# Kernel optimization log

Measured on AMD Instinct MI355X. Metric: run time of the kernel, lower is better.

Reference implementation:

```python
import jax, jax.numpy as jnp
import numpy as np
import math

B, LQ, LK = 8, 1024, 1024
DQ = DK = DV = DOUT = 512
H = 8
DH = DOUT // H
EPS = 1e-5


def _ln(x, g, b):
    m = jnp.mean(x, -1, keepdims=True)
    var = jnp.mean((x - m) ** 2, -1, keepdims=True)
    return (x - m) * jax.lax.rsqrt(var + EPS) * g + b


def setup_inputs() -> dict:
    key = jax.random.key(0)
    ks = jax.random.split(key, 13)
    s = 0.02
    return {
        "q": jax.random.normal(ks[0], (B, LQ, DQ), jnp.float32),
        "k": jax.random.normal(ks[1], (B, LK, DK), jnp.float32),
        "v": jax.random.normal(ks[2], (B, LK, DV), jnp.float32),
        "mask": jax.random.randint(ks[3], (B, LK), 0, 2) > 0,  # True = masked
        "Wq": jax.random.normal(ks[4], (DOUT, DQ), jnp.float32) * s,
        "Wk": jax.random.normal(ks[5], (DOUT, DK), jnp.float32) * s,
        "Wv": jax.random.normal(ks[6], (DOUT, DV), jnp.float32) * s,
        "Wo": jax.random.normal(ks[7], (DOUT, DOUT), jnp.float32) * s,
        "bo": jnp.zeros((DOUT,), jnp.float32),
        "g1": jnp.ones((DOUT,), jnp.float32),
        "b1": jnp.zeros((DOUT,), jnp.float32),
        "g2": jnp.ones((DOUT,), jnp.float32),
        "b2": jnp.zeros((DOUT,), jnp.float32),
    }


def reference(q, k, v, mask, Wq, Wk, Wv, Wo, bo, g1, b1, g2, b2):
    qp = q @ Wq.T  # [B,Lq,D]
    kp = k @ Wk.T  # [B,Lk,D]
    vp = v @ Wv.T  # [B,Lk,D]

    # split heads: chunk(num_heads, -1) -> head h = contiguous slice of size DH
    qh = qp.reshape(B, LQ, H, DH)
    kh = kp.reshape(B, LK, H, DH)
    vh = vp.reshape(B, LK, H, DH)

    # NOTE: module divides by sqrt(dim_out), not sqrt(head_dim)
    logits = jnp.einsum("bqhd,bkhd->bhqk", qh, kh) / math.sqrt(DOUT)
    logits = jnp.where(mask[:, None, None, :], -jnp.inf, logits)
    A = jax.nn.softmax(logits, axis=-1)
    A = jnp.where(jnp.isnan(A), 0.0, A)  # masked_fill(isnan, 0)

    attn = jnp.einsum("bhqk,bkhd->bqhd", A, vh).reshape(B, LQ, DOUT)

    out = _ln(qp + attn, g1, b1)
    out = _ln(out + jax.nn.relu(out @ Wo.T + bo), g2, b2)
    return out
```

## Files before the change

kernel.cpp:

```cpp
#include <hip/hip_runtime.h>
#include <math.h>
#include <stdint.h>

#define NB 8
#define SEQ 1024
#define DMODEL 512
#define NH 8
#define HD 64
#define R_TOT (NB * SEQ)

typedef __attribute__((ext_vector_type(8))) short bf16x8;
typedef __attribute__((ext_vector_type(4))) float f32x4;

__device__ __forceinline__ short f2b(float x) {
    uint32_t u = __float_as_uint(x);
    u += 0x7FFF + ((u >> 16) & 1);
    return (short)(u >> 16);
}
__device__ __forceinline__ float b2f(short s) {
    return __uint_as_float(((uint32_t)(uint16_t)s) << 16);
}
__device__ __forceinline__ uint32_t cvtpk_bf16(float lo, float hi) {
    uint32_t r;
    asm("v_cvt_pk_bf16_f32 %0, %1, %2" : "=v"(r) : "v"(lo), "v"(hi));
    return r;
}
__device__ __forceinline__ float exp2_hw(float x) {
    float r;
    asm("v_exp_f32 %0, %1" : "=v"(r) : "v"(x));
    return r;
}

#define GLD_LDS16(g, l)                                                        \
    __builtin_amdgcn_global_load_lds(                                          \
        (const __attribute__((address_space(1))) uint32_t*)(g),                \
        (__attribute__((address_space(3))) uint32_t*)(l), 16, 0, 0)

__device__ __forceinline__ void xcd_swizzle(int& bx, int& by, int& bz) {
    const int gx = gridDim.x, gy = gridDim.y;
    const int nwg = gx * gy * gridDim.z;
    int id = (blockIdx.z * gy + blockIdx.y) * gx + blockIdx.x;
    int lg = (id & 7) * (nwg >> 3) + (id >> 3);
    bx = lg % gx;
    int tmp = lg / gx;
    by = tmp % gy;
    bz = tmp / gy;
}

#define N4B (R_TOT * DMODEL / 4)
#define N4W (DMODEL * DMODEL / 4)

__global__ __launch_bounds__(256)
void cvt_all(const float* __restrict__ q, const float* __restrict__ k, const float* __restrict__ v,
             const float* __restrict__ wq, const float* __restrict__ wk,
             const float* __restrict__ wv, const float* __restrict__ wo,
             short* dq, short* dk, short* dv, short* dwq, short* dwk, short* dwv, short* dwo)
{
    long i = (long)blockIdx.x * 256 + threadIdx.x;
    const float* s; short* d; long off;
    if (i < (long)N4B)          { s = q;  d = dq;  off = i; }
    else if (i < 2L * N4B)      { s = k;  d = dk;  off = i - N4B; }
    else if (i < 3L * N4B)      { s = v;  d = dv;  off = i - 2L * N4B; }
    else {
        long j = i - 3L * N4B;
        int  w = (int)(j >> 16);
        off = j & (N4W - 1);
        s = (w == 0) ? wq : (w == 1) ? wk : (w == 2) ? wv : wo;
        d = (w == 0) ? dwq : (w == 1) ? dwk : (w == 2) ? dwv : dwo;
    }
    float4 x = ((const float4*)s)[off];
    short4 o;
    o.x = f2b(x.x); o.y = f2b(x.y); o.z = f2b(x.z); o.w = f2b(x.w);
    ((short4*)d)[off] = o;
}

#define GBM 128
#define GBN 64
#define GBK 64

__device__ __forceinline__ void gemm_core(
    const short* __restrict__ A, const short* __restrict__ Bm,
    const float* __restrict__ bias, short* __restrict__ C,
    int N, int m0, int n0, int relu, float oscale,
    short (*As)[GBM * GBK], short (*Bs)[GBN * GBK])
{
    const int tid = threadIdx.x;
    const int l   = tid & 63, w = tid >> 6;
    const int l15 = l & 15,  l4 = l >> 4;
    const int wrow = w >> 1, wcol = w & 1;
    const int K = 512;

    f32x4 acc[4][2] = {};

    auto stageA = [&](int t, int buf) {
        #pragma unroll
        for (int j = 0; j < 4; ++j) {
            int ch  = tid + j * 256;
            int row = ch >> 3;
            int so  = (((ch & 7) * 16) ^ ((row & 7) << 4)) >> 1;
            GLD_LDS16(A + (size_t)(m0 + row) * K + t * GBK + so, &As[buf][ch * 8]);
        }
    };
    auto stageB = [&](int t, int buf) {
        #pragma unroll
        for (int j = 0; j < 2; ++j) {
            int ch  = tid + j * 256;
            int row = ch >> 3;
            int so  = (((ch & 7) * 16) ^ ((row & 7) << 4)) >> 1;
            GLD_LDS16(Bm + (size_t)(n0 + row) * K + t * GBK + so, &Bs[buf][ch * 8]);
        }
    };

    stageA(0, 0); stageB(0, 0);
    __syncthreads();

    for (int t = 0; t < 8; ++t) {
        const int cur = t & 1;
        if (t + 1 < 8) { stageA(t + 1, cur ^ 1); stageB(t + 1, cur ^ 1); }
        __builtin_amdgcn_s_setprio(1);
        #pragma unroll
        for (int kk = 0; kk < 2; ++kk) {
            bf16x8 af[4], bfr[2];
            #pragma unroll
            for (int mi = 0; mi < 4; ++mi) {
                int row = wrow * 64 + mi * 16 + l15;
                af[mi] = *(const bf16x8*)((char*)&As[cur][row * GBK] +
                                          ((kk * 64 + l4 * 16) ^ ((row & 7) << 4)));
            }
            #pragma unroll
            for (int ni = 0; ni < 2; ++ni) {
                int row = wcol * 32 + ni * 16 + l15;
                bfr[ni] = *(const bf16x8*)((char*)&Bs[cur][row * GBK] +
                                           ((kk * 64 + l4 * 16) ^ ((row & 7) << 4)));
            }
            #pragma unroll
            for (int mi = 0; mi < 4; ++mi)
                #pragma unroll
                for (int ni = 0; ni < 2; ++ni)
                    acc[mi][ni] = __builtin_amdgcn_mfma_f32_16x16x32_bf16(af[mi], bfr[ni], acc[mi][ni], 0, 0, 0);
        }
        __builtin_amdgcn_s_setprio(0);
        __syncthreads();
    }

    #pragma unroll
    for (int mi = 0; mi < 4; ++mi) {
        #pragma unroll
        for (int ni = 0; ni < 2; ++ni) {
            int col = n0 + wcol * 32 + ni * 16 + l15;
            float bb = bias ? bias[col] : 0.0f;
            #pragma unroll
            for (int r = 0; r < 4; ++r) {
                int row = m0 + wrow * 64 + mi * 16 + l4 * 4 + r;
                float vv = (acc[mi][ni][r] + bb) * oscale;
                if (relu) vv = fmaxf(vv, 0.0f);
                C[(size_t)row * N + col] = f2b(vv);
            }
        }
    }
}

__global__ __launch_bounds__(256)
void proj3(const short* __restrict__ qb, const short* __restrict__ kb,
           const short* __restrict__ vb, const short* __restrict__ wq,
           const short* __restrict__ wv,
           short* __restrict__ qpb, short* __restrict__ vtb, float kscale)
{
    __shared__ short As[2][GBM * GBK];
    __shared__ short Bs[2][GBN * GBK];
    const size_t WSZ  = (size_t)DMODEL * DMODEL;
    const size_t SLOT = (size_t)R_TOT * DMODEL;

    int id = blockIdx.x;
    int lg = (id & 7) * 192 + (id >> 3);

    const short *A, *Bm; short* C; int N, m0, n0; float os = 1.0f;
    if (lg < 1024) {
        int bz  = lg >> 9;
        int rem = lg & 511;
        m0 = (rem >> 3) * GBM;
        n0 = (rem & 7) * GBN;
        A  = bz ? kb : qb;
        Bm = wq + bz * WSZ;
        C  = qpb + bz * SLOT;
        N  = DMODEL;
        os = bz ? kscale : 1.0f;
    } else {
        int r2  = lg - 1024;
        int b   = r2 >> 6;
        int rem = r2 & 63;
        m0 = (rem >> 4) * GBM;
        n0 = (rem & 15) * GBN;
        A  = wv;
        Bm = vb + (long)b * SEQ * DMODEL;
        C  = vtb + (long)b * DMODEL * SEQ;
        N  = SEQ;
    }
    gemm_core(A, Bm, nullptr, C, N, m0, n0, 0, os, As, Bs);
}

__global__ __launch_bounds__(256)
void outproj(const short* __restrict__ y, const short* __restrict__ wo,
             const float* __restrict__ bias, short* __restrict__ z)
{
    __shared__ short As[2][GBM * GBK];
    __shared__ short Bs[2][GBN * GBK];
    int bx, by, bz;
    xcd_swizzle(bx, by, bz);
    gemm_core(y, wo, bias, z, DMODEL, by * GBM, bx * GBN, 1, 1.0f, As, Bs);
}

__global__ __launch_bounds__(512)
void attn_mfma8(const short* __restrict__ qp, const short* __restrict__ kp,
                const short* __restrict__ vt, const int* __restrict__ mask,
                short* __restrict__ attn)
{
    __shared__ short Kb[2][2][64 * 64];
    __shared__ short Vb[2][2][64 * 64];
    __shared__ __align__(16) char Ps[8 * 2048];

    const int tid = threadIdx.x;
    const int l   = tid & 63, w = tid >> 6;
    const int l15 = l & 15,  l4 = l >> 4;
    int qb_, h, b;
    xcd_swizzle(qb_, h, b);
    const int qrow = qb_ * 128 + w * 16 + l15;
    const size_t baseqk = ((size_t)b * SEQ) * DMODEL + h * HD;
    const size_t basev  = ((size_t)b * DMODEL + h * HD) * SEQ;

    const int ch  = tid;
    const int row = ch >> 3;
    const int so  = ((((ch & 7) * 16) ^ ((row & 7) << 4)) >> 1);
    const short* kph = kp + baseqk;
    const short* vth = vt + basev;
    const int*   mrow = mask + b * SEQ;

#define STAGE(t, bufi) do {                                                                   \
        GLD_LDS16(kph + (size_t)((t) * 128 + row) * DMODEL + so,      &Kb[bufi][0][ch * 8]);  \
        GLD_LDS16(kph + (size_t)((t) * 128 + 64 + row) * DMODEL + so, &Kb[bufi][1][ch * 8]);  \
        GLD_LDS16(vth + (size_t)row * SEQ + (t) * 128 + so,           &Vb[bufi][0][ch * 8]);  \
        GLD_LDS16(vth + (size_t)row * SEQ + (t) * 128 + 64 + so,      &Vb[bufi][1][ch * 8]);  \
    } while (0)

    const int swk   = (l15 & 7) << 4;
    const int kOff0 = l15 * 128 + ((l4 * 16) ^ swk);
    const int kOff1 = l15 * 128 + ((64 + l4 * 16) ^ swk);
    int pwOff[4];
    #pragma unroll
    for (int c = 0; c < 4; ++c)
        pwOff[c] = (l15 * 128 + c * 32 + l4 * 8) ^ swk;
    const int prOff0 = (l15 * 128 + l4 * 16) ^ swk;
    const int prOff1 = (l15 * 128 + 64 + l4 * 16) ^ swk;

    bf16x8 qf0, qf1;
    {
        const short* qr = qp + baseqk + (size_t)qrow * DMODEL + l4 * 8;
        qf0 = *(const bf16x8*)qr;
        qf1 = *(const bf16x8*)(qr + 32);
    }
    const bf16x8 ones = {0x3F80, 0x3F80, 0x3F80, 0x3F80, 0x3F80, 0x3F80, 0x3F80, 0x3F80};

    STAGE(0, 0);
    __syncthreads();

    f32x4 oacc[4] = {};
    f32x4 osum = {};
    char* myPs = Ps + w * 2048;

    for (int t = 0; t < 8; ++t) {
        const int cur = t & 1;
        if (t < 7) STAGE(t + 1, cur ^ 1);

        #pragma unroll
        for (int hf = 0; hf < 2; ++hf) {
            f32x4 s[4];
            __builtin_amdgcn_s_setprio(1);
            #pragma unroll
            for (int c = 0; c < 4; ++c) {
                const char* kbase = (const char*)&Kb[cur][hf][0] + c * 2048;
                bf16x8 kf0 = *(const bf16x8*)(kbase + kOff0);
                bf16x8 kf1 = *(const bf16x8*)(kbase + kOff1);
                f32x4 zz = {};
                zz = __builtin_amdgcn_mfma_f32_16x16x32_bf16(kf0, qf0, zz, 0, 0, 0);
                zz = __builtin_amdgcn_mfma_f32_16x16x32_bf16(kf1, qf1, zz, 0, 0, 0);
                s[c] = zz;
            }
            __builtin_amdgcn_s_setprio(0);

            float p[16];
            #pragma unroll
            for (int c = 0; c < 4; ++c) {
                int4 mi = *(const int4*)&mrow[t * 128 + hf * 64 + c * 16 + l4 * 4];
                p[c * 4 + 0] = exp2_hw(mi.x ? -1.0e30f : s[c][0]);
                p[c * 4 + 1] = exp2_hw(mi.y ? -1.0e30f : s[c][1]);
                p[c * 4 + 2] = exp2_hw(mi.z ? -1.0e30f : s[c][2]);
                p[c * 4 + 3] = exp2_hw(mi.w ? -1.0e30f : s[c][3]);
            }

            #pragma unroll
            for (int c = 0; c < 4; ++c) {
                uint2 u;
                u.x = cvtpk_bf16(p[c * 4 + 0], p[c * 4 + 1]);
                u.y = cvtpk_bf16(p[c * 4 + 2], p[c * 4 + 3]);
                *(uint2*)(myPs + pwOff[c]) = u;
            }
            bf16x8 pf0 = *(const bf16x8*)(myPs + prOff0);
            bf16x8 pf1 = *(const bf16x8*)(myPs + prOff1);

            __builtin_amdgcn_s_setprio(1);
            osum = __builtin_amdgcn_mfma_f32_16x16x32_bf16(ones, pf0, osum, 0, 0, 0);
            osum = __builtin_amdgcn_mfma_f32_16x16x32_bf16(ones, pf1, osum, 0, 0, 0);
            #pragma unroll
            for (int db = 0; db < 4; ++db) {
                const char* vbase = (const char*)&Vb[cur][hf][0] + db * 2048;
                bf16x8 vf0 = *(const bf16x8*)(vbase + kOff0);
                bf16x8 vf1 = *(const bf16x8*)(vbase + kOff1);
                oacc[db] = __builtin_amdgcn_mfma_f32_16x16x32_bf16(vf0, pf0, oacc[db], 0, 0, 0);
                oacc[db] = __builtin_amdgcn_mfma_f32_16x16x32_bf16(vf1, pf1, oacc[db], 0, 0, 0);
            }
            __builtin_amdgcn_s_setprio(0);
        }
        __syncthreads();
    }
#undef STAGE

    float inv = (osum[0] > 0.0f) ? 1.0f / osum[0] : 0.0f;
    #pragma unroll
    for (int db = 0; db < 4; ++db) {
        short4 o;
        o.x = f2b(oacc[db][0] * inv);
        o.y = f2b(oacc[db][1] * inv);
        o.z = f2b(oacc[db][2] * inv);
        o.w = f2b(oacc[db][3] * inv);
        *(short4*)(attn + baseqk + (size_t)qrow * DMODEL + db * 16 + l4 * 4) = o;
    }
}

__global__ __launch_bounds__(256)
void add_ln_b(const short* __restrict__ A, const short* __restrict__ Bv,
              const float* __restrict__ g, const float* __restrict__ beta,
              short* __restrict__ outb, float* __restrict__ outf)
{
    const int row = blockIdx.x;
    const int tid = threadIdx.x;
    const size_t off = (size_t)row * DMODEL;
    short2 a2 = *(const short2*)&A[off + tid * 2];
    short2 c2 = *(const short2*)&Bv[off + tid * 2];
    float x0 = b2f(a2.x) + b2f(c2.x);
    float x1 = b2f(a2.y) + b2f(c2.y);
    float s  = x0 + x1;
    float sq = x0 * x0 + x1 * x1;
    #pragma unroll
    for (int o = 1; o < 64; o <<= 1) {
        s  += __shfl_xor(s,  o);
        sq += __shfl_xor(sq, o);
    }
    __shared__ float ls[4], lq[4];
    const int w = tid >> 6;
    if ((tid & 63) == 0) { ls[w] = s; lq[w] = sq; }
    __syncthreads();
    s  = ls[0] + ls[1] + ls[2] + ls[3];
    sq = lq[0] + lq[1] + lq[2] + lq[3];
    const float mean = s * (1.0f / DMODEL);
    const float var  = sq * (1.0f / DMODEL) - mean * mean;
    const float rs   = rsqrtf(var + 1e-5f);
    const int c0 = tid * 2, c1 = tid * 2 + 1;
    float y0 = (x0 - mean) * rs * g[c0] + beta[c0];
    float y1 = (x1 - mean) * rs * g[c1] + beta[c1];
    if (outb) {
        short2 o; o.x = f2b(y0); o.y = f2b(y1);
        *(short2*)&outb[off + tid * 2] = o;
    } else {
        float2 o; o.x = y0; o.y = y1;
        *(float2*)&outf[off + tid * 2] = o;
    }
}

extern "C" void kernel_launch(void* const* d_in, const int* in_sizes, int n_in,
                              void* d_out, int out_size, void* d_ws, size_t ws_size,
                              hipStream_t stream)
{
    const float* q    = (const float*)d_in[0];
    const float* k    = (const float*)d_in[1];
    const float* v    = (const float*)d_in[2];
    const int*   mask = (const int*)  d_in[3];
    const float* Wq   = (const float*)d_in[4];
    const float* Wk   = (const float*)d_in[5];
    const float* Wv   = (const float*)d_in[6];
    const float* Wo   = (const float*)d_in[7];
    const float* bo   = (const float*)d_in[8];
    const float* g1   = (const float*)d_in[9];
    const float* b1   = (const float*)d_in[10];
    const float* g2   = (const float*)d_in[11];
    const float* bt2  = (const float*)d_in[12];
    float* out = (float*)d_out;

    short* ws = (short*)d_ws;
    const size_t WSZ  = (size_t)DMODEL * DMODEL;
    const size_t SLOT = (size_t)R_TOT * DMODEL;
    short* wq  = ws;
    short* wk  = ws + WSZ;
    short* wv  = ws + 2 * WSZ;
    short* wo  = ws + 3 * WSZ;
    short* qb  = ws + 4 * WSZ;
    short* kb  = qb + SLOT;
    short* vb  = kb + SLOT;
    short* qpb = vb + SLOT;
    short* kpb = qpb + SLOT;
    short* vtb = kpb + SLOT;
    short* at  = qb;
    short* y   = kb;
    short* z   = vb;

    const int nCvtBlocks = (3 * N4B + 4 * N4W) / 256;
    cvt_all<<<nCvtBlocks, 256, 0, stream>>>(q, k, v, Wq, Wk, Wv, Wo,
                                            qb, kb, vb, wq, wk, wv, wo);

    const float kscale = 0.06375871530f;

    proj3<<<1536, 256, 0, stream>>>(qb, kb, vb, wq, wv, qpb, vtb, kscale);

    attn_mfma8<<<dim3(SEQ / 128, NH, NB), 512, 0, stream>>>(qpb, kpb, vtb, mask, at);

    add_ln_b<<<R_TOT, 256, 0, stream>>>(qpb, at, g1, b1, y, nullptr);

    outproj<<<dim3(DMODEL / GBN, R_TOT / GBM, 1), 256, 0, stream>>>(y, wo, bo, z);

    add_ln_b<<<R_TOT, 256, 0, stream>>>(y, z, g2, bt2, nullptr, out);
}
```

Baseline: 93.45 us.

## Fuse residual adds into attention and outproj epilogues, use one-wave-per-row LayerNorm

```diff
diff --git a/kernel.cpp b/kernel.cpp
--- a/kernel.cpp
+++ b/kernel.cpp
@@ -80,7 +80,8 @@
 
 __device__ __forceinline__ void gemm_core(
     const short* __restrict__ A, const short* __restrict__ Bm,
-    const float* __restrict__ bias, short* __restrict__ C,
+    const float* __restrict__ bias, const short* __restrict__ resid,
+    short* __restrict__ C,
     int N, int m0, int n0, int relu, float oscale,
     short (*As)[GBM * GBK], short (*Bs)[GBN * GBK])
 {
@@ -154,6 +155,7 @@
                 int row = m0 + wrow * 64 + mi * 16 + l4 * 4 + r;
                 float vv = (acc[mi][ni][r] + bb) * oscale;
                 if (relu) vv = fmaxf(vv, 0.0f);
+                if (resid) vv += b2f(resid[(size_t)row * N + col]);
                 C[(size_t)row * N + col] = f2b(vv);
             }
         }
@@ -196,7 +198,7 @@
         C  = vtb + (long)b * DMODEL * SEQ;
         N  = SEQ;
     }
-    gemm_core(A, Bm, nullptr, C, N, m0, n0, 0, os, As, Bs);
+    gemm_core(A, Bm, nullptr, nullptr, C, N, m0, n0, 0, os, As, Bs);
 }
 
 __global__ __launch_bounds__(256)
@@ -207,11 +209,11 @@
     __shared__ short Bs[2][GBN * GBK];
     int bx, by, bz;
     xcd_swizzle(bx, by, bz);
-    gemm_core(y, wo, bias, z, DMODEL, by * GBM, bx * GBN, 1, 1.0f, As, Bs);
+    gemm_core(y, wo, bias, y, z, DMODEL, by * GBM, bx * GBN, 1, 1.0f, As, Bs);
 }
 
 __global__ __launch_bounds__(512)
-void attn_mfma8(const short* __restrict__ qp, const short* __restrict__ kp,
+void attn_mfma9(const short* __restrict__ qp, const short* __restrict__ kp,
                 const short* __restrict__ vt, const int* __restrict__ mask,
                 short* __restrict__ attn)
 {
@@ -271,6 +273,13 @@
         const int cur = t & 1;
         if (t < 7) STAGE(t + 1, cur ^ 1);
 
+        int4 mreg[2][4];
+        #pragma unroll
+        for (int hf = 0; hf < 2; ++hf)
+            #pragma unroll
+            for (int c = 0; c < 4; ++c)
+                mreg[hf][c] = *(const int4*)&mrow[t * 128 + hf * 64 + c * 16 + l4 * 4];
+
         #pragma unroll
         for (int hf = 0; hf < 2; ++hf) {
             f32x4 s[4];
@@ -290,7 +299,7 @@
             float p[16];
             #pragma unroll
             for (int c = 0; c < 4; ++c) {
-                int4 mi = *(const int4*)&mrow[t * 128 + hf * 64 + c * 16 + l4 * 4];
+                int4 mi = mreg[hf][c];
                 p[c * 4 + 0] = exp2_hw(mi.x ? -1.0e30f : s[c][0]);
                 p[c * 4 + 1] = exp2_hw(mi.y ? -1.0e30f : s[c][1]);
                 p[c * 4 + 2] = exp2_hw(mi.z ? -1.0e30f : s[c][2]);
@@ -327,52 +336,61 @@
     float inv = (osum[0] > 0.0f) ? 1.0f / osum[0] : 0.0f;
     #pragma unroll
     for (int db = 0; db < 4; ++db) {
+        const size_t eoff = baseqk + (size_t)qrow * DMODEL + db * 16 + l4 * 4;
+        short4 qv = *(const short4*)(qp + eoff);
         short4 o;
-        o.x = f2b(oacc[db][0] * inv);
-        o.y = f2b(oacc[db][1] * inv);
-        o.z = f2b(oacc[db][2] * inv);
-        o.w = f2b(oacc[db][3] * inv);
-        *(short4*)(attn + baseqk + (size_t)qrow * DMODEL + db * 16 + l4 * 4) = o;
+        o.x = f2b(oacc[db][0] * inv + b2f(qv.x));
+        o.y = f2b(oacc[db][1] * inv + b2f(qv.y));
+        o.z = f2b(oacc[db][2] * inv + b2f(qv.z));
+        o.w = f2b(oacc[db][3] * inv + b2f(qv.w));
+        *(short4*)(attn + eoff) = o;
     }
 }
 
 __global__ __launch_bounds__(256)
-void add_ln_b(const short* __restrict__ A, const short* __restrict__ Bv,
-              const float* __restrict__ g, const float* __restrict__ beta,
-              short* __restrict__ outb, float* __restrict__ outf)
-{
-    const int row = blockIdx.x;
-    const int tid = threadIdx.x;
-    const size_t off = (size_t)row * DMODEL;
-    short2 a2 = *(const short2*)&A[off + tid * 2];
-    short2 c2 = *(const short2*)&Bv[off + tid * 2];
-    float x0 = b2f(a2.x) + b2f(c2.x);
-    float x1 = b2f(a2.y) + b2f(c2.y);
-    float s  = x0 + x1;
-    float sq = x0 * x0 + x1 * x1;
+void ln_one(const short* __restrict__ X, const float* __restrict__ g,
+            const float* __restrict__ beta, short* __restrict__ outb,
+            float* __restrict__ outf)
+{
+    const int row  = blockIdx.x * 4 + (threadIdx.x >> 6);
+    const int lane = threadIdx.x & 63;
+    const size_t off = (size_t)row * DMODEL + lane * 8;
+    bf16x8 xv = *(const bf16x8*)&X[off];
+    float x[8], s = 0.0f, sq = 0.0f;
+    #pragma unroll
+    for (int i = 0; i < 8; ++i) {
+        x[i] = b2f(xv[i]);
+        s += x[i];
+        sq += x[i] * x[i];
+    }
     #pragma unroll
     for (int o = 1; o < 64; o <<= 1) {
         s  += __shfl_xor(s,  o);
         sq += __shfl_xor(sq, o);
     }
-    __shared__ float ls[4], lq[4];
-    const int w = tid >> 6;
-    if ((tid & 63) == 0) { ls[w] = s; lq[w] = sq; }
-    __syncthreads();
-    s  = ls[0] + ls[1] + ls[2] + ls[3];
-    sq = lq[0] + lq[1] + lq[2] + lq[3];
     const float mean = s * (1.0f / DMODEL);
     const float var  = sq * (1.0f / DMODEL) - mean * mean;
     const float rs   = rsqrtf(var + 1e-5f);
-    const int c0 = tid * 2, c1 = tid * 2 + 1;
-    float y0 = (x0 - mean) * rs * g[c0] + beta[c0];
-    float y1 = (x1 - mean) * rs * g[c1] + beta[c1];
+    float4 g0 = *(const float4*)&g[lane * 8];
+    float4 g1 = *(const float4*)&g[lane * 8 + 4];
+    float4 b0 = *(const float4*)&beta[lane * 8];
+    float4 b1 = *(const float4*)&beta[lane * 8 + 4];
+    float gg[8] = {g0.x, g0.y, g0.z, g0.w, g1.x, g1.y, g1.z, g1.w};
+    float bb[8] = {b0.x, b0.y, b0.z, b0.w, b1.x, b1.y, b1.z, b1.w};
+    float y[8];
+    #pragma unroll
+    for (int i = 0; i < 8; ++i)
+        y[i] = (x[i] - mean) * rs * gg[i] + bb[i];
     if (outb) {
-        short2 o; o.x = f2b(y0); o.y = f2b(y1);
-        *(short2*)&outb[off + tid * 2] = o;
+        bf16x8 o;
+        #pragma unroll
+        for (int i = 0; i < 8; ++i) o[i] = f2b(y[i]);
+        *(bf16x8*)&outb[off] = o;
     } else {
-        float2 o; o.x = y0; o.y = y1;
-        *(float2*)&outf[off + tid * 2] = o;
+        float4 o0 = {y[0], y[1], y[2], y[3]};
+        float4 o1 = {y[4], y[5], y[6], y[7]};
+        *(float4*)&outf[off] = o0;
+        *(float4*)&outf[off + 4] = o1;
     }
 }
 
@@ -420,11 +438,11 @@
 
     proj3<<<1536, 256, 0, stream>>>(qb, kb, vb, wq, wv, qpb, vtb, kscale);
 
-    attn_mfma8<<<dim3(SEQ / 128, NH, NB), 512, 0, stream>>>(qpb, kpb, vtb, mask, at);
-
-    add_ln_b<<<R_TOT, 256, 0, stream>>>(qpb, at, g1, b1, y, nullptr);
+    attn_mfma9<<<dim3(SEQ / 128, NH, NB), 512, 0, stream>>>(qpb, kpb, vtb, mask, at);
+
+    ln_one<<<R_TOT / 4, 256, 0, stream>>>(at, g1, b1, y, nullptr);
 
     outproj<<<dim3(DMODEL / GBN, R_TOT / GBM, 1), 256, 0, stream>>>(y, wo, bo, z);
 
-    add_ln_b<<<R_TOT, 256, 0, stream>>>(y, z, g2, bt2, nullptr, out);
-}
+    ln_one<<<R_TOT / 4, 256, 0, stream>>>(z, g2, bt2, nullptr, out);
+}
```

Result: no change. 92.79 us (median of 3 runs) (-0.7%).
